# Optimization experiments

Measured on AMD Instinct MI355X. Metric: run time of the kernel, lower is better.

Reference implementation:

```python
import jax, jax.numpy as jnp
import numpy as np

D_MODEL = 1024
N_HEADS = 8
EDGE_HID = 512
N_EDGE_CLS = 18
N_NODE_CLS = 18
MAX_NODES = 15


def setup_inputs() -> dict:
    key = jax.random.key(0)
    ks = jax.random.split(key, 24)
    B, T, L, D = 32, 4, 1024, D_MODEL
    N = MAX_NODES
    s = 0.02
    visual_feats = jax.random.normal(ks[0], (B, T, L, D), jnp.float32)
    nodes = jax.random.randint(ks[1], (B, N), 0, N_NODE_CLS, dtype=jnp.int32)
    bboxes = jax.random.uniform(ks[2], (B, N, 4), jnp.float32)
    # embedding table; padding_idx=-1 -> last row zeroed (unused due to clamp)
    emb = (jax.random.normal(ks[3], (N_NODE_CLS + 1, D)) * s).at[-1].set(0.0)
    Wb = jax.random.normal(ks[4], (D, 4)) * s
    bb = jnp.zeros((D,), jnp.float32)
    Wq = jax.random.normal(ks[5], (D, D)) * s
    bq = jnp.zeros((D,), jnp.float32)
    Wk = jax.random.normal(ks[6], (D, D)) * s
    bk = jnp.zeros((D,), jnp.float32)
    Wv = jax.random.normal(ks[7], (D, D)) * s
    bv = jnp.zeros((D,), jnp.float32)
    Wo = jax.random.normal(ks[8], (D, D)) * s
    bo = jnp.zeros((D,), jnp.float32)
    W1 = jax.random.normal(ks[9], (EDGE_HID, 2 * D)) * s
    b1 = jnp.zeros((EDGE_HID,), jnp.float32)
    W2 = jax.random.normal(ks[10], (N_EDGE_CLS, EDGE_HID)) * s
    b2 = jnp.zeros((N_EDGE_CLS,), jnp.float32)
    Wh1 = jax.random.normal(ks[11], (256, D)) * s
    bh1 = jnp.zeros((256,), jnp.float32)
    Wh2 = jax.random.normal(ks[12], (1, 256)) * s
    bh2 = jnp.zeros((1,), jnp.float32)
    return dict(visual_feats=visual_feats, nodes=nodes, bboxes=bboxes, emb=emb,
                Wb=Wb, bb=bb, Wq=Wq, bq=bq, Wk=Wk, bk=bk, Wv=Wv, bv=bv,
                Wo=Wo, bo=bo, W1=W1, b1=b1, W2=W2, b2=b2,
                Wh1=Wh1, bh1=bh1, Wh2=Wh2, bh2=bh2)


def reference(visual_feats, nodes, bboxes, emb, Wb, bb, Wq, bq, Wk, bk, Wv, bv,
              Wo, bo, W1, b1, W2, b2, Wh1, bh1, Wh2, bh2):
    B, T, L, D = visual_feats.shape
    H = N_HEADS
    Hd = D // H
    v_f = visual_feats[:, -1]  # (B, L, D)
    n_emb = emb[jnp.maximum(nodes, 0)]            # (B, N, D)
    query = n_emb + bboxes @ Wb.T + bb            # (B, N, D)
    N = query.shape[1]
    # multi-head cross-attention (query=nodes, key/value=visual tokens)
    q = (query @ Wq.T + bq).reshape(B, N, H, Hd)
    k = (v_f @ Wk.T + bk).reshape(B, L, H, Hd)
    v = (v_f @ Wv.T + bv).reshape(B, L, H, Hd)
    scores = jnp.einsum('bnhd,blhd->bhnl', q, k) / jnp.sqrt(jnp.float32(Hd))
    attn = jax.nn.softmax(scores, axis=-1)
    ctx = jnp.einsum('bhnl,blhd->bnhd', attn, v).reshape(B, N, D)
    enriched = ctx @ Wo.T + bo                    # (B, N, D)
    pad = nodes == -1                             # all False here
    clean = jnp.where(pad[..., None], 0.0, enriched)
    # edge MLP: decompose first Linear over the concat into two half matmuls
    h_i = enriched @ W1[:, :D].T                  # (B, N, E)
    h_j = enriched @ W1[:, D:].T                  # (B, N, E)
    pair = jax.nn.relu(h_i[:, :, None, :] + h_j[:, None, :, :] + b1)  # (B,N,N,E)
    edge_logits = pair @ W2.T + b2                # (B, N, N, 18)
    valid = jnp.maximum(jnp.sum(~pad, axis=1, keepdims=True), 1).astype(enriched.dtype)
    gfeat = jnp.sum(clean, axis=1) / valid        # (B, D)
    energy = (jax.nn.relu(gfeat @ Wh1.T + bh1) @ Wh2.T + bh2).squeeze(-1)  # (B,)
    return edge_logits, energy
```

## Files before the change

kernel.cpp:

```cpp
#include <hip/hip_runtime.h>


typedef __attribute__((ext_vector_type(8))) short bf16x8;
typedef __attribute__((ext_vector_type(4))) float f32x4;

__device__ __forceinline__ unsigned short f2bf(float f) {
    unsigned int u = __float_as_uint(f);
    u = u + 0x7FFFu + ((u >> 16) & 1u);
    return (unsigned short)(u >> 16);
}

template <bool OUTBF>
__global__ __launch_bounds__(256) void bfgemm_k(
    const unsigned short* __restrict__ A, const unsigned short* __restrict__ B,
    void* __restrict__ Cv, int M, long sA, long sB, long sC)
{
    const int b  = blockIdx.z;
    const int m0 = blockIdx.y * 64;
    const int n0 = blockIdx.x * 128;
    const unsigned short* Ab = A + b * sA;
    const unsigned short* Bb = B + b * sB;

    __shared__ __align__(16) unsigned short As[64 * 32];
    __shared__ __align__(16) unsigned short Bs[128 * 32];

    const int t    = threadIdx.x;
    const int lane = t & 63;
    const int w    = t >> 6;
    const int wm   = w >> 1, wn = w & 1;

    f32x4 acc[2][4] = {};

    const int ar = t >> 2;
    const int ac = (t & 3) * 8;

    for (int k0 = 0; k0 < 1024; k0 += 32) {
        uint4 av  = *(const uint4*)(Ab + (long)(m0 + ar) * 1024 + k0 + ac);
        uint4 bv0 = *(const uint4*)(Bb + (long)(n0 + ar) * 1024 + k0 + ac);
        uint4 bv1 = *(const uint4*)(Bb + (long)(n0 + 64 + ar) * 1024 + k0 + ac);
        __syncthreads();
        *(uint4*)&As[t * 8]        = av;
        *(uint4*)&Bs[t * 8]        = bv0;
        *(uint4*)&Bs[2048 + t * 8] = bv1;
        __syncthreads();

        const int krow = (lane >> 4) * 8;
        bf16x8 af[2], bf[4];
#pragma unroll
        for (int fi = 0; fi < 2; ++fi)
            af[fi] = *(const bf16x8*)&As[(wm * 32 + fi * 16 + (lane & 15)) * 32 + krow];
#pragma unroll
        for (int fj = 0; fj < 4; ++fj)
            bf[fj] = *(const bf16x8*)&Bs[(wn * 64 + fj * 16 + (lane & 15)) * 32 + krow];
#pragma unroll
        for (int fi = 0; fi < 2; ++fi)
#pragma unroll
            for (int fj = 0; fj < 4; ++fj)
                acc[fi][fj] = __builtin_amdgcn_mfma_f32_16x16x32_bf16(
                    af[fi], bf[fj], acc[fi][fj], 0, 0, 0);
    }

    const int rbase = (lane >> 4) * 4;
    const int cn    = n0 + wn * 64 + (lane & 15);
#pragma unroll
    for (int fi = 0; fi < 2; ++fi) {
        const int mb = m0 + wm * 32 + fi * 16 + rbase;
#pragma unroll
        for (int r = 0; r < 4; ++r) {
            const int m = mb + r;
            if (m < M) {
#pragma unroll
                for (int fj = 0; fj < 4; ++fj) {
                    if constexpr (OUTBF)
                        ((unsigned short*)Cv)[b * sC + (long)m * 1024 + cn + fj * 16]
                            = f2bf(acc[fi][fj][r]);
                    else
                        ((float*)Cv)[b * sC + (long)m * 1024 + cn + fj * 16]
                            = acc[fi][fj][r];
                }
            }
        }
    }
}

template <int OM>
__global__ __launch_bounds__(256) void pgemm_k(
    const unsigned short* __restrict__ A, const unsigned short* __restrict__ B,
    const float* __restrict__ bias, float* __restrict__ C,
    unsigned short* __restrict__ Cbf,
    int M, int K, int lda, int ldb, int ldc)
{
    const int m0 = blockIdx.y * 64;
    const int n0 = blockIdx.x * 64;

    __shared__ __align__(16) unsigned short As[64 * 32];
    __shared__ __align__(16) unsigned short Bs[64 * 32];

    const int t    = threadIdx.x;
    const int lane = t & 63;
    const int w    = t >> 6;
    const int wm   = w >> 1, wn = w & 1;
    const int lm   = lane & 15, lg = lane >> 4;

    const int ar = t >> 2;
    const int ac = (t & 3) * 8;

    f32x4 acc[2][2] = {};

    for (int k0 = 0; k0 < K; k0 += 32) {
        uint4 av = *(const uint4*)(A + (long)(m0 + ar) * lda + k0 + ac);
        uint4 bv = *(const uint4*)(B + (long)(n0 + ar) * ldb + k0 + ac);
        __syncthreads();
        *(uint4*)&As[t * 8] = av;
        *(uint4*)&Bs[t * 8] = bv;
        __syncthreads();

        const int krow = lg * 8 & 24;
        bf16x8 af[2], bf[2];
#pragma unroll
        for (int fi = 0; fi < 2; ++fi)
            af[fi] = *(const bf16x8*)&As[(wm * 32 + fi * 16 + lm) * 32 + krow];
#pragma unroll
        for (int fj = 0; fj < 2; ++fj)
            bf[fj] = *(const bf16x8*)&Bs[(wn * 32 + fj * 16 + lm) * 32 + krow];
#pragma unroll
        for (int fi = 0; fi < 2; ++fi)
#pragma unroll
            for (int fj = 0; fj < 2; ++fj)
                acc[fi][fj] = __builtin_amdgcn_mfma_f32_16x16x32_bf16(
                    af[fi], bf[fj], acc[fi][fj], 0, 0, 0);
    }

    const int rbase = lg * 4;
#pragma unroll
    for (int fi = 0; fi < 2; ++fi) {
        const int mb = m0 + wm * 32 + fi * 16 + rbase;
#pragma unroll
        for (int r = 0; r < 4; ++r) {
            const int m = mb + r;
            if (m < M) {
#pragma unroll
                for (int fj = 0; fj < 2; ++fj) {
                    const int n = n0 + wn * 32 + fj * 16 + lm;
                    float v = acc[fi][fj][r];
                    if (bias) v += bias[n];
                    if constexpr (OM != 2) C[(long)m * ldc + n] = v;
                    if constexpr (OM >= 1) Cbf[(long)m * ldc + n] = f2bf(v);
                }
            }
        }
    }
}

__global__ __launch_bounds__(256) void qw_k(
    const unsigned short* __restrict__ qbf, const unsigned short* __restrict__ WkT,
    unsigned short* __restrict__ qW, float scale)
{
    const int z = blockIdx.y;
    const int b = z >> 3, h = z & 7;
    const int w = threadIdx.x >> 6, lane = threadIdx.x & 63;
    const int lm = lane & 15, lg = lane >> 4;
    const int n0w = blockIdx.x * 256 + w * 64;

    const unsigned short* Ar = qbf + (long)(b * 15 + lm) * 1024 + h * 128 + lg * 8;
    const unsigned short* Br = WkT + (long)(n0w + lm) * 1024 + h * 128 + lg * 8;

    bf16x8 af[4];
#pragma unroll
    for (int ks = 0; ks < 4; ++ks) af[ks] = *(const bf16x8*)(Ar + ks * 32);

    f32x4 acc[4] = {};
#pragma unroll
    for (int fj = 0; fj < 4; ++fj) {
#pragma unroll
        for (int ks = 0; ks < 4; ++ks) {
            bf16x8 bf = *(const bf16x8*)(Br + (long)fj * 16 * 1024 + ks * 32);
            acc[fj] = __builtin_amdgcn_mfma_f32_16x16x32_bf16(af[ks], bf, acc[fj], 0, 0, 0);
        }
    }

#pragma unroll
    for (int r = 0; r < 4; ++r) {
        const int m = lg * 4 + r;
        if (m < 15) {
#pragma unroll
            for (int fj = 0; fj < 4; ++fj)
                qW[(long)b * 131072 + (long)(m * 8 + h) * 1024 + n0w + fj * 16 + lm]
                    = f2bf(acc[fj][r] * scale);
        }
    }
}

__global__ __launch_bounds__(256) void ctx_k(
    const unsigned short* __restrict__ cf, const unsigned short* __restrict__ Wvb,
    const float* __restrict__ bv, unsigned short* __restrict__ ctx)
{
    const int z = blockIdx.x;
    const int b = z >> 3, h = z & 7;
    const int w = threadIdx.x >> 6, lane = threadIdx.x & 63;
    const int lm = lane & 15, lg = lane >> 4;

    const unsigned short* Ar = cf + (long)b * 122880 + (long)(lm * 8 + h) * 1024 + lg * 8;
    const unsigned short* Br = Wvb + (long)(h * 128 + w * 32 + lm) * 1024 + lg * 8;

    f32x4 acc[2] = {};
    for (int k0 = 0; k0 < 1024; k0 += 32) {
        bf16x8 af = *(const bf16x8*)(Ar + k0);
        bf16x8 b0 = *(const bf16x8*)(Br + k0);
        bf16x8 b1 = *(const bf16x8*)(Br + 16 * 1024 + k0);
        acc[0] = __builtin_amdgcn_mfma_f32_16x16x32_bf16(af, b0, acc[0], 0, 0, 0);
        acc[1] = __builtin_amdgcn_mfma_f32_16x16x32_bf16(af, b1, acc[1], 0, 0, 0);
    }

#pragma unroll
    for (int r = 0; r < 4; ++r) {
        const int m = lg * 4 + r;
        if (m < 15) {
#pragma unroll
            for (int fj = 0; fj < 2; ++fj) {
                const int gcol = h * 128 + w * 32 + fj * 16 + lm;
                ctx[(long)(b * 15 + m) * 1024 + gcol] = f2bf(acc[fj][r] + bv[gcol]);
            }
        }
    }
}

__global__ __launch_bounds__(256) void cvtW_k(
    const float* __restrict__ Wq, const float* __restrict__ Wo,
    const float* __restrict__ Wv, const float* __restrict__ W1,
    unsigned short* __restrict__ dWq, unsigned short* __restrict__ dWo,
    unsigned short* __restrict__ dWv, unsigned short* __restrict__ dW1r)
{
    const int which = blockIdx.y;
    const int i = blockIdx.x * 256 + threadIdx.x;
    const float* s;
    unsigned short* d;
    if (which == 3) {
        const int flat = i * 4, n = flat >> 10, k = flat & 1023;
        s = (n < 512) ? W1 + (long)n * 2048 + k : W1 + (long)(n - 512) * 2048 + 1024 + k;
        d = dW1r + flat;
    } else {
        s = (which == 0 ? Wq : which == 1 ? Wo : Wv) + (long)i * 4;
        d = (which == 0 ? dWq : which == 1 ? dWo : dWv) + (long)i * 4;
    }
    float4 v = *(const float4*)s;
    ushort4 o;
    o.x = f2bf(v.x); o.y = f2bf(v.y); o.z = f2bf(v.z); o.w = f2bf(v.w);
    *(ushort4*)d = o;
}

__global__ __launch_bounds__(256) void cvtT_k(
    const float* __restrict__ src, unsigned short* __restrict__ dst)
{
    const int d0 = blockIdx.y * 64, e0 = blockIdx.x * 64;
    __shared__ unsigned short tile[64][72];
    const int t = threadIdx.x;
    const int r0 = t >> 4, c0 = (t & 15) * 4;
#pragma unroll
    for (int rr = 0; rr < 4; ++rr) {
        const int r = r0 + rr * 16;
        float4 v = *(const float4*)&src[(long)(d0 + r) * 1024 + e0 + c0];
        tile[r][c0 + 0] = f2bf(v.x); tile[r][c0 + 1] = f2bf(v.y);
        tile[r][c0 + 2] = f2bf(v.z); tile[r][c0 + 3] = f2bf(v.w);
    }
    __syncthreads();
#pragma unroll
    for (int rr = 0; rr < 4; ++rr) {
        const int idx = rr * 256 + t;
        const int e = idx >> 4, c4 = (idx & 15) * 4;
        ushort4 o;
        o.x = tile[c4 + 0][e]; o.y = tile[c4 + 1][e];
        o.z = tile[c4 + 2][e]; o.w = tile[c4 + 3][e];
        *(ushort4*)&dst[(long)(e0 + e) * 1024 + d0 + c4] = o;
    }
}

__global__ __launch_bounds__(256) void cvt_k(
    const float* __restrict__ vf, unsigned short* __restrict__ vbf,
    unsigned short* __restrict__ vbfT)
{
    const int b  = blockIdx.z;
    const int e0 = blockIdx.x * 64;
    const int l0 = blockIdx.y * 64;
    const float* src = vf + (long)b * 4194304;
    __shared__ unsigned short tile[64][72];
    const int t = threadIdx.x;
    const int r0 = t >> 4, c0 = (t & 15) * 4;
#pragma unroll
    for (int rr = 0; rr < 4; ++rr) {
        const int r = r0 + rr * 16;
        float4 v = *(const float4*)&src[(long)(l0 + r) * 1024 + e0 + c0];
        ushort4 o;
        o.x = f2bf(v.x); o.y = f2bf(v.y); o.z = f2bf(v.z); o.w = f2bf(v.w);
        tile[r][c0 + 0] = o.x; tile[r][c0 + 1] = o.y;
        tile[r][c0 + 2] = o.z; tile[r][c0 + 3] = o.w;
        *(ushort4*)&vbf[(long)b * 1048576 + (long)(l0 + r) * 1024 + e0 + c0] = o;
    }
    __syncthreads();
#pragma unroll
    for (int rr = 0; rr < 4; ++rr) {
        const int idx = rr * 256 + t;
        const int e   = idx >> 4;
        const int c4  = (idx & 15) * 4;
        ushort4 o;
        o.x = tile[c4 + 0][e]; o.y = tile[c4 + 1][e];
        o.z = tile[c4 + 2][e]; o.w = tile[c4 + 3][e];
        *(ushort4*)&vbfT[(long)b * 1048576 + (long)(e0 + e) * 1024 + l0 + c4] = o;
    }
}

__global__ __launch_bounds__(256) void build_query_k(
    const int* __restrict__ nodes, const float* __restrict__ bboxes,
    const float* __restrict__ emb, const float* __restrict__ Wb,
    const float* __restrict__ bb, unsigned short* __restrict__ qbf)
{
    const int blk = blockIdx.x;
    const int node = nodes[blk];
    const int idx = node < 0 ? 0 : node;
    const float4 bx = *(const float4*)&bboxes[blk * 4];
    const float* er = emb + (long)idx * 1024;
    for (int d = threadIdx.x; d < 1024; d += 256) {
        const float4 w = *(const float4*)&Wb[d * 4];
        qbf[(long)blk * 1024 + d] = f2bf(
            er[d] + bb[d] + bx.x * w.x + bx.y * w.y + bx.z * w.z + bx.w * w.w);
    }
}

__global__ __launch_bounds__(256) void softmax_k(
    const float* __restrict__ sc, unsigned short* __restrict__ attn)
{
    __shared__ float red[4];
    const int blk = blockIdx.x;
    const int b = blk / 120, r = blk % 120;
    const float* p = sc + (long)blk * 1024;
    const int t = threadIdx.x;
    float4 v = *(const float4*)&p[t * 4];

    float m = fmaxf(fmaxf(v.x, v.y), fmaxf(v.z, v.w));
#pragma unroll
    for (int o = 32; o; o >>= 1) m = fmaxf(m, __shfl_xor(m, o));
    if ((t & 63) == 0) red[t >> 6] = m;
    __syncthreads();
    m = fmaxf(fmaxf(red[0], red[1]), fmaxf(red[2], red[3]));
    __syncthreads();

    v.x = __expf(v.x - m); v.y = __expf(v.y - m);
    v.z = __expf(v.z - m); v.w = __expf(v.w - m);
    float s = v.x + v.y + v.z + v.w;
#pragma unroll
    for (int o = 32; o; o >>= 1) s += __shfl_xor(s, o);
    if ((t & 63) == 0) red[t >> 6] = s;
    __syncthreads();
    s = red[0] + red[1] + red[2] + red[3];
    const float inv = 1.0f / s;
    ushort4 o;
    o.x = f2bf(v.x * inv); o.y = f2bf(v.y * inv);
    o.z = f2bf(v.z * inv); o.w = f2bf(v.w * inv);
    *(ushort4*)&attn[(long)(b * 128 + r) * 1024 + t * 4] = o;
}

__global__ __launch_bounds__(320) void edge_k(
    const float* __restrict__ hh, const float* __restrict__ b1,
    const float* __restrict__ W2, const float* __restrict__ b2,
    float* __restrict__ out)
{
    const int b = blockIdx.x, i = blockIdx.y;
    const int t = threadIdx.x;
    __shared__ float hiS[256];
    __shared__ float b1S[256];
    __shared__ float hjS[15][257];
    __shared__ float w2S[18][257];
    const int j = t / 18, c = t % 18;
    float acc = 0.0f;

    for (int u0 = 0; u0 < 512; u0 += 256) {
        __syncthreads();
        if (t < 64) {
            float4 v = *(const float4*)&hh[(long)(b * 15 + i) * 1024 + u0 + t * 4];
            hiS[t * 4 + 0] = v.x; hiS[t * 4 + 1] = v.y;
            hiS[t * 4 + 2] = v.z; hiS[t * 4 + 3] = v.w;
        } else if (t < 128) {
            const int tt = t - 64;
            float4 v = *(const float4*)&b1[u0 + tt * 4];
            b1S[tt * 4 + 0] = v.x; b1S[tt * 4 + 1] = v.y;
            b1S[tt * 4 + 2] = v.z; b1S[tt * 4 + 3] = v.w;
        }
        for (int x = t; x < 960; x += 320) {
            const int r = x >> 6, cc = (x & 63) * 4;
            float4 v = *(const float4*)&hh[(long)(b * 15 + r) * 1024 + 512 + u0 + cc];
            hjS[r][cc + 0] = v.x; hjS[r][cc + 1] = v.y;
            hjS[r][cc + 2] = v.z; hjS[r][cc + 3] = v.w;
        }
        for (int x = t; x < 1152; x += 320) {
            const int r = x >> 6, cc = (x & 63) * 4;
            float4 v = *(const float4*)&W2[(long)r * 512 + u0 + cc];
            w2S[r][cc + 0] = v.x; w2S[r][cc + 1] = v.y;
            w2S[r][cc + 2] = v.z; w2S[r][cc + 3] = v.w;
        }
        __syncthreads();
        if (t < 270) {
            for (int u = 0; u < 256; ++u) {
                float p = hiS[u] + hjS[j][u] + b1S[u];
                p = p > 0.0f ? p : 0.0f;
                acc += p * w2S[c][u];
            }
        }
    }
    if (t < 270)
        out[((long)(b * 15 + i) * 15 + j) * 18 + c] = acc + b2[c];
}

__global__ __launch_bounds__(256) void energy1_k(
    const float* __restrict__ enr, const int* __restrict__ nodes,
    float* __restrict__ gfeat)
{
    const int b = blockIdx.y;
    const int e = blockIdx.x * 256 + threadIdx.x;
    int cnt = 0;
#pragma unroll
    for (int n = 0; n < 15; ++n) cnt += (nodes[b * 15 + n] != -1) ? 1 : 0;
    const float inv_valid = 1.0f / fmaxf((float)cnt, 1.0f);
    float s = 0.0f;
#pragma unroll
    for (int n = 0; n < 15; ++n) {
        const bool ok = nodes[b * 15 + n] != -1;
        s += ok ? enr[(long)(b * 15 + n) * 1024 + e] : 0.0f;
    }
    gfeat[b * 1024 + e] = s * inv_valid;
}

__global__ __launch_bounds__(256) void energy2_k(
    const float* __restrict__ gfeat, const float* __restrict__ Wh1,
    const float* __restrict__ bh1, const float* __restrict__ Wh2,
    float* __restrict__ hidr)
{
    const int b  = blockIdx.y;
    const int u0 = blockIdx.x * 16;
    const int t = threadIdx.x;
    __shared__ float gf[1024];
    {
        float4 v = *(const float4*)&gfeat[b * 1024 + t * 4];
        gf[t * 4 + 0] = v.x; gf[t * 4 + 1] = v.y;
        gf[t * 4 + 2] = v.z; gf[t * 4 + 3] = v.w;
    }
    __syncthreads();
    const int wave = t >> 6, lane = t & 63;
#pragma unroll
    for (int r = 0; r < 4; ++r) {
        const int u = u0 + wave * 4 + r;
        float s = 0.0f;
#pragma unroll
        for (int e0 = 0; e0 < 1024; e0 += 64)
            s += gf[e0 + lane] * Wh1[(long)u * 1024 + e0 + lane];
#pragma unroll
        for (int o = 32; o; o >>= 1) s += __shfl_xor(s, o);
        if (lane == 0)
            hidr[b * 256 + u] = fmaxf(s + bh1[u], 0.0f) * Wh2[u];
    }
}

__global__ __launch_bounds__(256) void energy3_k(
    const float* __restrict__ hidr, const float* __restrict__ bh2,
    float* __restrict__ out)
{
    const int b = blockIdx.x;
    const int t = threadIdx.x;
    __shared__ float red[4];
    float v = hidr[b * 256 + t];
#pragma unroll
    for (int o = 32; o; o >>= 1) v += __shfl_xor(v, o);
    if ((t & 63) == 0) red[t >> 6] = v;
    __syncthreads();
    if (t == 0) out[129600 + b] = red[0] + red[1] + red[2] + red[3] + bh2[0];
}

extern "C" void kernel_launch(void* const* d_in, const int* in_sizes, int n_in,
                              void* d_out, int out_size, void* d_ws, size_t ws_size,
                              hipStream_t stream)
{
    const float* visual = (const float*)d_in[0];
    const int*   nodes  = (const int*)  d_in[1];
    const float* bboxes = (const float*)d_in[2];
    const float* emb    = (const float*)d_in[3];
    const float* Wb     = (const float*)d_in[4];
    const float* bb     = (const float*)d_in[5];
    const float* Wq     = (const float*)d_in[6];
    const float* bq     = (const float*)d_in[7];
    const float* Wk     = (const float*)d_in[8];
    const float* Wv     = (const float*)d_in[10];
    const float* bv     = (const float*)d_in[11];
    const float* Wo     = (const float*)d_in[12];
    const float* bo     = (const float*)d_in[13];
    const float* W1     = (const float*)d_in[14];
    const float* b1     = (const float*)d_in[15];
    const float* W2     = (const float*)d_in[16];
    const float* b2     = (const float*)d_in[17];
    const float* Wh1    = (const float*)d_in[18];
    const float* bh1    = (const float*)d_in[19];
    const float* Wh2    = (const float*)d_in[20];
    const float* bh2    = (const float*)d_in[21];

    float* out = (float*)d_out;
    float* ws  = (float*)d_ws;

    unsigned short* query_bf = (unsigned short*)(ws);
    unsigned short* q_bf     = (unsigned short*)(ws + 131072);
    float* scores = ws + 262144;
    unsigned short* ctxf_bf  = (unsigned short*)(ws + 4194304);
    unsigned short* ctx_bf   = (unsigned short*)(ws + 6160384);
    float* enr    = ws + 6422528;
    unsigned short* enr_bf   = (unsigned short*)(ws + 6914048);
    float* hh     = ws + 7176192;
    unsigned short* Wq_bf  = (unsigned short*)(ws + 7667712);
    unsigned short* Wo_bf  = (unsigned short*)(ws + 8192000);
    unsigned short* Wv_bf  = (unsigned short*)(ws + 8716288);
    unsigned short* W1r_bf = (unsigned short*)(ws + 9240576);
    unsigned short* WkT_bf = (unsigned short*)(ws + 9764864);
    unsigned short* qW_bf   = (unsigned short*)(ws + 10289152);
    unsigned short* attn_bf = (unsigned short*)(ws + 12386304);
    unsigned short* v_bf    = (unsigned short*)(ws + 14483456);
    unsigned short* v_bfT   = (unsigned short*)(ws + 31260672);
    float* gfeat  = ws + 48037888;
    float* hidr   = ws + 48070656;

    const float inv_sqrt_hd = 0.08838834764831845f;
    const float* v_f = visual + 3 * 1048576;

    build_query_k<<<480, 256, 0, stream>>>(nodes, bboxes, emb, Wb, bb, query_bf);
    cvt_k<<<dim3(16, 16, 32), 256, 0, stream>>>(v_f, v_bf, v_bfT);
    cvtW_k<<<dim3(1024, 4), 256, 0, stream>>>(Wq, Wo, Wv, W1, Wq_bf, Wo_bf, Wv_bf, W1r_bf);
    cvtT_k<<<dim3(16, 16), 256, 0, stream>>>(Wk, WkT_bf);

    pgemm_k<2><<<dim3(16, 8), 256, 0, stream>>>(
        query_bf, Wq_bf, bq, nullptr, q_bf, 480, 1024, 1024, 1024, 1024);

    qw_k<<<dim3(4, 256), 256, 0, stream>>>(q_bf, WkT_bf, qW_bf, inv_sqrt_hd);

    bfgemm_k<false><<<dim3(8, 2, 32), 256, 0, stream>>>(
        qW_bf, v_bf, scores, 120, 131072, 1048576, 122880);

    softmax_k<<<3840, 256, 0, stream>>>(scores, attn_bf);

    bfgemm_k<true><<<dim3(8, 2, 32), 256, 0, stream>>>(
        attn_bf, v_bfT, ctxf_bf, 120, 131072, 1048576, 122880);

    ctx_k<<<256, 256, 0, stream>>>(ctxf_bf, Wv_bf, bv, ctx_bf);

    pgemm_k<1><<<dim3(16, 8), 256, 0, stream>>>(
        ctx_bf, Wo_bf, bo, enr, enr_bf, 480, 1024, 1024, 1024, 1024);

    pgemm_k<0><<<dim3(16, 8), 256, 0, stream>>>(
        enr_bf, W1r_bf, nullptr, hh, nullptr, 480, 1024, 1024, 1024, 1024);

    edge_k<<<dim3(32, 15), 320, 0, stream>>>(hh, b1, W2, b2, out);

    energy1_k<<<dim3(4, 32), 256, 0, stream>>>(enr, nodes, gfeat);
    energy2_k<<<dim3(16, 32), 256, 0, stream>>>(gfeat, Wh1, bh1, Wh2, hidr);
    energy3_k<<<32, 256, 0, stream>>>(hidr, bh2, out);
}
```

Before: 245.5 us.

## Use direct global-to-LDS loads in GEMMs and merge small prep/energy kernels

The bf16 GEMM kernels now stage tiles with global_load_lds, copying straight into shared memory instead of going through registers. The four weight-conversion and query-building kernels are merged into one launch. The first two energy kernels are fused, with each block recomputing its gfeat row in shared memory. This cuts launch count and register staging, at the cost of redundant gfeat reductions and no explicit wait on the asynchronous LDS loads beyond __syncthreads.

```diff
diff --git a/kernel.cpp b/kernel.cpp
--- a/kernel.cpp
+++ b/kernel.cpp
@@ -8,6 +8,13 @@
     unsigned int u = __float_as_uint(f);
     u = u + 0x7FFFu + ((u >> 16) & 1u);
     return (unsigned short)(u >> 16);
+}
+
+__device__ __forceinline__ void gload_lds16(const void* g, void* l) {
+    __builtin_amdgcn_global_load_lds(
+        (const __attribute__((address_space(1))) void*)g,
+        (__attribute__((address_space(3))) void*)l,
+        16, 0, 0);
 }
 
 template <bool OUTBF>
@@ -34,14 +41,18 @@
     const int ar = t >> 2;
     const int ac = (t & 3) * 8;
 
+    unsigned short* AsW  = As + w * 512;
+    unsigned short* BsW0 = Bs + w * 512;
+    unsigned short* BsW1 = Bs + 2048 + w * 512;
+    const unsigned short* ga  = Ab + (long)(m0 + ar) * 1024 + ac;
+    const unsigned short* gb0 = Bb + (long)(n0 + ar) * 1024 + ac;
+    const unsigned short* gb1 = Bb + (long)(n0 + 64 + ar) * 1024 + ac;
+
     for (int k0 = 0; k0 < 1024; k0 += 32) {
-        uint4 av  = *(const uint4*)(Ab + (long)(m0 + ar) * 1024 + k0 + ac);
-        uint4 bv0 = *(const uint4*)(Bb + (long)(n0 + ar) * 1024 + k0 + ac);
-        uint4 bv1 = *(const uint4*)(Bb + (long)(n0 + 64 + ar) * 1024 + k0 + ac);
-        __syncthreads();
-        *(uint4*)&As[t * 8]        = av;
-        *(uint4*)&Bs[t * 8]        = bv0;
-        *(uint4*)&Bs[2048 + t * 8] = bv1;
+        __syncthreads();
+        gload_lds16(ga  + k0, AsW);
+        gload_lds16(gb0 + k0, BsW0);
+        gload_lds16(gb1 + k0, BsW1);
         __syncthreads();
 
         const int krow = (lane >> 4) * 8;
@@ -107,12 +118,15 @@
 
     f32x4 acc[2][2] = {};
 
+    unsigned short* AsW = As + w * 512;
+    unsigned short* BsW = Bs + w * 512;
+    const unsigned short* ga = A + (long)(m0 + ar) * lda + ac;
+    const unsigned short* gb = B + (long)(n0 + ar) * ldb + ac;
+
     for (int k0 = 0; k0 < K; k0 += 32) {
-        uint4 av = *(const uint4*)(A + (long)(m0 + ar) * lda + k0 + ac);
-        uint4 bv = *(const uint4*)(B + (long)(n0 + ar) * ldb + k0 + ac);
-        __syncthreads();
-        *(uint4*)&As[t * 8] = av;
-        *(uint4*)&Bs[t * 8] = bv;
+        __syncthreads();
+        gload_lds16(ga + k0, AsW);
+        gload_lds16(gb + k0, BsW);
         __syncthreads();
 
         const int krow = lg * 8 & 24;
@@ -225,53 +239,71 @@
     }
 }
 
-__global__ __launch_bounds__(256) void cvtW_k(
+__global__ __launch_bounds__(256) void uber_cvt_k(
+    const int* __restrict__ nodes, const float* __restrict__ bboxes,
+    const float* __restrict__ emb, const float* __restrict__ Wb,
+    const float* __restrict__ bb, unsigned short* __restrict__ qbf,
     const float* __restrict__ Wq, const float* __restrict__ Wo,
     const float* __restrict__ Wv, const float* __restrict__ W1,
+    const float* __restrict__ Wk,
     unsigned short* __restrict__ dWq, unsigned short* __restrict__ dWo,
-    unsigned short* __restrict__ dWv, unsigned short* __restrict__ dW1r)
-{
-    const int which = blockIdx.y;
-    const int i = blockIdx.x * 256 + threadIdx.x;
-    const float* s;
-    unsigned short* d;
-    if (which == 3) {
-        const int flat = i * 4, n = flat >> 10, k = flat & 1023;
-        s = (n < 512) ? W1 + (long)n * 2048 + k : W1 + (long)(n - 512) * 2048 + 1024 + k;
-        d = dW1r + flat;
+    unsigned short* __restrict__ dWv, unsigned short* __restrict__ dW1r,
+    unsigned short* __restrict__ dWkT)
+{
+    __shared__ unsigned short tile[64][72];
+    const int bid = blockIdx.x;
+    const int t = threadIdx.x;
+
+    if (bid < 4096) {
+        const int which = bid >> 10;
+        const int i = (bid & 1023) * 256 + t;
+        const float* s;
+        unsigned short* d;
+        if (which == 3) {
+            const int flat = i * 4, n = flat >> 10, k = flat & 1023;
+            s = (n < 512) ? W1 + (long)n * 2048 + k
+                          : W1 + (long)(n - 512) * 2048 + 1024 + k;
+            d = dW1r + flat;
+        } else {
+            s = (which == 0 ? Wq : which == 1 ? Wo : Wv) + (long)i * 4;
+            d = (which == 0 ? dWq : which == 1 ? dWo : dWv) + (long)i * 4;
+        }
+        float4 v = *(const float4*)s;
+        ushort4 o;
+        o.x = f2bf(v.x); o.y = f2bf(v.y); o.z = f2bf(v.z); o.w = f2bf(v.w);
+        *(ushort4*)d = o;
+    } else if (bid < 4352) {
+        const int tl = bid - 4096;
+        const int d0 = (tl >> 4) * 64, e0 = (tl & 15) * 64;
+        const int r0 = t >> 4, c0 = (t & 15) * 4;
+#pragma unroll
+        for (int rr = 0; rr < 4; ++rr) {
+            const int r = r0 + rr * 16;
+            float4 v = *(const float4*)&Wk[(long)(d0 + r) * 1024 + e0 + c0];
+            tile[r][c0 + 0] = f2bf(v.x); tile[r][c0 + 1] = f2bf(v.y);
+            tile[r][c0 + 2] = f2bf(v.z); tile[r][c0 + 3] = f2bf(v.w);
+        }
+        __syncthreads();
+#pragma unroll
+        for (int rr = 0; rr < 4; ++rr) {
+            const int idx = rr * 256 + t;
+            const int e = idx >> 4, c4 = (idx & 15) * 4;
+            ushort4 o;
+            o.x = tile[c4 + 0][e]; o.y = tile[c4 + 1][e];
+            o.z = tile[c4 + 2][e]; o.w = tile[c4 + 3][e];
+            *(ushort4*)&dWkT[(long)(e0 + e) * 1024 + d0 + c4] = o;
+        }
     } else {
-        s = (which == 0 ? Wq : which == 1 ? Wo : Wv) + (long)i * 4;
-        d = (which == 0 ? dWq : which == 1 ? dWo : dWv) + (long)i * 4;
-    }
-    float4 v = *(const float4*)s;
-    ushort4 o;
-    o.x = f2bf(v.x); o.y = f2bf(v.y); o.z = f2bf(v.z); o.w = f2bf(v.w);
-    *(ushort4*)d = o;
-}
-
-__global__ __launch_bounds__(256) void cvtT_k(
-    const float* __restrict__ src, unsigned short* __restrict__ dst)
-{
-    const int d0 = blockIdx.y * 64, e0 = blockIdx.x * 64;
-    __shared__ unsigned short tile[64][72];
-    const int t = threadIdx.x;
-    const int r0 = t >> 4, c0 = (t & 15) * 4;
-#pragma unroll
-    for (int rr = 0; rr < 4; ++rr) {
-        const int r = r0 + rr * 16;
-        float4 v = *(const float4*)&src[(long)(d0 + r) * 1024 + e0 + c0];
-        tile[r][c0 + 0] = f2bf(v.x); tile[r][c0 + 1] = f2bf(v.y);
-        tile[r][c0 + 2] = f2bf(v.z); tile[r][c0 + 3] = f2bf(v.w);
-    }
-    __syncthreads();
-#pragma unroll
-    for (int rr = 0; rr < 4; ++rr) {
-        const int idx = rr * 256 + t;
-        const int e = idx >> 4, c4 = (idx & 15) * 4;
-        ushort4 o;
-        o.x = tile[c4 + 0][e]; o.y = tile[c4 + 1][e];
-        o.z = tile[c4 + 2][e]; o.w = tile[c4 + 3][e];
-        *(ushort4*)&dst[(long)(e0 + e) * 1024 + d0 + c4] = o;
+        const int blk = bid - 4352;
+        const int node = nodes[blk];
+        const int idx = node < 0 ? 0 : node;
+        const float4 bx = *(const float4*)&bboxes[blk * 4];
+        const float* er = emb + (long)idx * 1024;
+        for (int d = t; d < 1024; d += 256) {
+            const float4 w = *(const float4*)&Wb[d * 4];
+            qbf[(long)blk * 1024 + d] = f2bf(
+                er[d] + bb[d] + bx.x * w.x + bx.y * w.y + bx.z * w.z + bx.w * w.w);
+        }
     }
 }
 
@@ -306,23 +338,6 @@
         o.x = tile[c4 + 0][e]; o.y = tile[c4 + 1][e];
         o.z = tile[c4 + 2][e]; o.w = tile[c4 + 3][e];
         *(ushort4*)&vbfT[(long)b * 1048576 + (long)(e0 + e) * 1024 + l0 + c4] = o;
-    }
-}
-
-__global__ __launch_bounds__(256) void build_query_k(
-    const int* __restrict__ nodes, const float* __restrict__ bboxes,
-    const float* __restrict__ emb, const float* __restrict__ Wb,
-    const float* __restrict__ bb, unsigned short* __restrict__ qbf)
-{
-    const int blk = blockIdx.x;
-    const int node = nodes[blk];
-    const int idx = node < 0 ? 0 : node;
-    const float4 bx = *(const float4*)&bboxes[blk * 4];
-    const float* er = emb + (long)idx * 1024;
-    for (int d = threadIdx.x; d < 1024; d += 256) {
-        const float4 w = *(const float4*)&Wb[d * 4];
-        qbf[(long)blk * 1024 + d] = f2bf(
-            er[d] + bb[d] + bx.x * w.x + bx.y * w.y + bx.z * w.z + bx.w * w.w);
     }
 }
 
@@ -410,40 +425,31 @@
         out[((long)(b * 15 + i) * 15 + j) * 18 + c] = acc + b2[c];
 }
 
-__global__ __launch_bounds__(256) void energy1_k(
+__global__ __launch_bounds__(256) void energy12_k(
     const float* __restrict__ enr, const int* __restrict__ nodes,
-    float* __restrict__ gfeat)
-{
-    const int b = blockIdx.y;
-    const int e = blockIdx.x * 256 + threadIdx.x;
-    int cnt = 0;
-#pragma unroll
-    for (int n = 0; n < 15; ++n) cnt += (nodes[b * 15 + n] != -1) ? 1 : 0;
-    const float inv_valid = 1.0f / fmaxf((float)cnt, 1.0f);
-    float s = 0.0f;
-#pragma unroll
-    for (int n = 0; n < 15; ++n) {
-        const bool ok = nodes[b * 15 + n] != -1;
-        s += ok ? enr[(long)(b * 15 + n) * 1024 + e] : 0.0f;
-    }
-    gfeat[b * 1024 + e] = s * inv_valid;
-}
-
-__global__ __launch_bounds__(256) void energy2_k(
-    const float* __restrict__ gfeat, const float* __restrict__ Wh1,
-    const float* __restrict__ bh1, const float* __restrict__ Wh2,
-    float* __restrict__ hidr)
+    const float* __restrict__ Wh1, const float* __restrict__ bh1,
+    const float* __restrict__ Wh2, float* __restrict__ hidr)
 {
     const int b  = blockIdx.y;
     const int u0 = blockIdx.x * 16;
     const int t = threadIdx.x;
     __shared__ float gf[1024];
-    {
-        float4 v = *(const float4*)&gfeat[b * 1024 + t * 4];
-        gf[t * 4 + 0] = v.x; gf[t * 4 + 1] = v.y;
-        gf[t * 4 + 2] = v.z; gf[t * 4 + 3] = v.w;
+
+    int cnt = 0;
+#pragma unroll
+    for (int n = 0; n < 15; ++n) cnt += (nodes[b * 15 + n] != -1) ? 1 : 0;
+    const float inv_valid = 1.0f / fmaxf((float)cnt, 1.0f);
+    for (int e = t; e < 1024; e += 256) {
+        float s = 0.0f;
+#pragma unroll
+        for (int n = 0; n < 15; ++n) {
+            const bool ok = nodes[b * 15 + n] != -1;
+            s += ok ? enr[(long)(b * 15 + n) * 1024 + e] : 0.0f;
+        }
+        gf[e] = s * inv_valid;
     }
     __syncthreads();
+
     const int wave = t >> 6, lane = t & 63;
 #pragma unroll
     for (int r = 0; r < 4; ++r) {
@@ -520,16 +526,15 @@
     unsigned short* attn_bf = (unsigned short*)(ws + 12386304);
     unsigned short* v_bf    = (unsigned short*)(ws + 14483456);
     unsigned short* v_bfT   = (unsigned short*)(ws + 31260672);
-    float* gfeat  = ws + 48037888;
     float* hidr   = ws + 48070656;
 
     const float inv_sqrt_hd = 0.08838834764831845f;
     const float* v_f = visual + 3 * 1048576;
 
-    build_query_k<<<480, 256, 0, stream>>>(nodes, bboxes, emb, Wb, bb, query_bf);
+    uber_cvt_k<<<4832, 256, 0, stream>>>(
+        nodes, bboxes, emb, Wb, bb, query_bf,
+        Wq, Wo, Wv, W1, Wk, Wq_bf, Wo_bf, Wv_bf, W1r_bf, WkT_bf);
     cvt_k<<<dim3(16, 16, 32), 256, 0, stream>>>(v_f, v_bf, v_bfT);
-    cvtW_k<<<dim3(1024, 4), 256, 0, stream>>>(Wq, Wo, Wv, W1, Wq_bf, Wo_bf, Wv_bf, W1r_bf);
-    cvtT_k<<<dim3(16, 16), 256, 0, stream>>>(Wk, WkT_bf);
 
     pgemm_k<2><<<dim3(16, 8), 256, 0, stream>>>(
         query_bf, Wq_bf, bq, nullptr, q_bf, 480, 1024, 1024, 1024, 1024);
@@ -554,7 +559,6 @@
 
     edge_k<<<dim3(32, 15), 320, 0, stream>>>(hh, b1, W2, b2, out);
 
-    energy1_k<<<dim3(4, 32), 256, 0, stream>>>(enr, nodes, gfeat);
-    energy2_k<<<dim3(16, 32), 256, 0, stream>>>(gfeat, Wh1, bh1, Wh2, hidr);
+    energy12_k<<<dim3(16, 32), 256, 0, stream>>>(enr, nodes, Wh1, bh1, Wh2, hidr);
     energy3_k<<<32, 256, 0, stream>>>(hidr, bh2, out);
 }
```

New measurement: 238.4 us. -2.9%, faster.
